# Kernel optimization log

Measured on AMD Instinct MI355X. Metric: run time of the kernel, lower is better.

The kernel has to match this reference:

```python
import jax, jax.numpy as jnp
import numpy as np
from jax import lax

COS_BASIS_NO = 24
SCALE = 6.0
SHIFT = 1.0


def make_kern_basis(T_no):
    # [24, T_no] raised-cosine log-time basis, matching the torch loop exactly
    i = jnp.arange(COS_BASIS_NO, dtype=jnp.float32)
    phi = (jnp.pi / 2.0) * i                                  # [24]
    x = jnp.arange(T_no, dtype=jnp.float32)
    raw = SCALE * jnp.log(x + SHIFT + 1e-7)                   # [T_no]
    basis = 0.5 * jnp.cos(raw[None, :] - phi[:, None]) + 0.5  # [24, T_no]
    inside = (raw[None, :] >= phi[:, None] - jnp.pi) & (raw[None, :] <= phi[:, None] + jnp.pi)
    return jnp.where(inside, basis, 0.0)


def causal_grouped_conv(x, kern, sub_no, T_no):
    # x: [B, sub_no, T], kern: [sub_no*hid, T_no] (already flipped like torch)
    # left-pad T_no-1 zeros == the torch zero-padded buffer; cross-correlation
    rhs = kern[:, None, :]  # OIH with I=1 per group
    return lax.conv_general_dilated(
        x, rhs, window_strides=(1,), padding=[(T_no - 1, 0)],
        feature_group_count=sub_no,
        dimension_numbers=("NCH", "OIH", "NCH"))


def setup_inputs() -> dict:
    key = jax.random.key(0)
    ks = jax.random.split(key, 10)
    B, T_data = 8, 5000
    sub_no, E_no, I_no, T_no, hid_no = 20, 2000, 200, 400, 16
    inp = {
        "S_e": jax.random.uniform(ks[0], (B, T_data, E_no), dtype=jnp.float32),
        "S_i": jax.random.uniform(ks[1], (B, T_data, I_no), dtype=jnp.float32),
        "E_scale": jnp.zeros((E_no,), jnp.float32),
        "I_scale": jnp.zeros((I_no,), jnp.float32),
        "W_e_layer1": jax.random.normal(ks[2], (sub_no * hid_no, COS_BASIS_NO), jnp.float32) * 0.01,
        "W_i_layer1": jax.random.normal(ks[3], (sub_no * hid_no, COS_BASIS_NO), jnp.float32) * 0.01,
        "W_layer2": jnp.full((sub_no, hid_no), -1.0, jnp.float32),
        "b_layer1": jnp.zeros((sub_no * hid_no,), jnp.float32),
        "C_syn_e_raw": jax.random.normal(ks[4], (sub_no, E_no), jnp.float32) * 0.01,
        "C_syn_i_raw": jax.random.normal(ks[5], (sub_no, I_no), jnp.float32) * 0.01,
        "V_o": jnp.zeros((1,), jnp.float32),
        "temp": jnp.asarray(1.0, jnp.float32),
        "T_no": T_no,
        "test": 1,
    }
    return inp


def reference(S_e, S_i, E_scale, I_scale, W_e_layer1, W_i_layer1, W_layer2,
              b_layer1, C_syn_e_raw, C_syn_i_raw, V_o, temp, T_no, test):
    sub_no = C_syn_e_raw.shape[0]
    hid_no = W_layer2.shape[1]
    B, T_data, _ = S_e.shape

    if test:
        C_syn_e = jax.nn.softmax(C_syn_e_raw / temp, axis=0)
        C_syn_i = jax.nn.softmax(C_syn_i_raw / temp, axis=0)
    else:
        eps = 1e-8
        ku, kv = jax.random.split(jax.random.key(42))
        u_e = jax.random.uniform(ku, C_syn_e_raw.shape, dtype=C_syn_e_raw.dtype)
        u_i = jax.random.uniform(kv, C_syn_i_raw.shape, dtype=C_syn_i_raw.dtype)
        g_e = -jnp.log(-jnp.log(u_e + eps) + eps)
        g_i = -jnp.log(-jnp.log(u_i + eps) + eps)
        C_syn_e = jax.nn.softmax((C_syn_e_raw + g_e) / temp, axis=0)
        C_syn_i = jax.nn.softmax((C_syn_i_raw + g_i) / temp, axis=0)

    # scale synapses and project onto subunits: [B,T,E] x [E,sub] -> [B,T,sub]
    syn_e = jnp.einsum("bte,se->bts", S_e * jnp.exp(E_scale)[None, None, :], C_syn_e)
    syn_i = jnp.einsum("bti,si->bts", S_i * jnp.exp(I_scale)[None, None, :], C_syn_i)

    kern_basis = make_kern_basis(T_no)                        # [24, T_no]
    ke = jnp.flip(W_e_layer1 @ kern_basis, axis=1)            # [sub*hid, T_no]
    ki = jnp.flip(W_i_layer1 @ kern_basis, axis=1)

    xe = jnp.transpose(syn_e, (0, 2, 1))                      # [B, sub, T]
    xi = jnp.transpose(syn_i, (0, 2, 1))
    conv_e = causal_grouped_conv(xe, ke, sub_no, T_no)        # [B, sub*hid, T]
    conv_i = causal_grouped_conv(xi, ki, sub_no, T_no)
    layer1 = jnp.tanh(conv_e + conv_i + b_layer1[None, :, None])

    # grouped 1x1 conv == per-subunit weighted reduction over hid
    h = layer1.reshape(B, sub_no, hid_no, T_data)
    sub_out = jnp.einsum("bshT,sh->bTs", h, jnp.exp(W_layer2))  # [B, T, sub]
    final = jnp.sum(sub_out, axis=-1) + V_o                    # [B, T]
    return final, sub_out, C_syn_e, C_syn_i
```

## Files before the change

kernel.cpp:

```cpp
#include <hip/hip_runtime.h>
#include <math.h>

#define PI_F 3.14159265358979323846f
#define BSTRIDE 404

__global__ __launch_bounds__(256) void prep_kernel(
    const float* __restrict__ Ce_raw, const float* __restrict__ Ci_raw,
    const float* __restrict__ Escale, const float* __restrict__ Iscale,
    const float* __restrict__ temp,
    float* __restrict__ CsT_e, float* __restrict__ CsT_i,
    float* __restrict__ basis,
    float* __restrict__ outCe, float* __restrict__ outCi)
{
    int id = blockIdx.x * 256 + threadIdx.x;
    if (id < 2000) {
        int e = id;
        float t = temp[0];
        float v[20];
        float m = -1e30f;
        #pragma unroll
        for (int s = 0; s < 20; ++s) { v[s] = Ce_raw[s * 2000 + e] / t; m = fmaxf(m, v[s]); }
        float sum = 0.f;
        #pragma unroll
        for (int s = 0; s < 20; ++s) { v[s] = expf(v[s] - m); sum += v[s]; }
        float inv = 1.f / sum;
        float sc = expf(Escale[e]);
        #pragma unroll
        for (int s = 0; s < 20; ++s) {
            float p = v[s] * inv;
            outCe[s * 2000 + e] = p;
            CsT_e[e * 20 + s] = p * sc;
        }
    } else if (id < 2200) {
        int e = id - 2000;
        float t = temp[0];
        float v[20];
        float m = -1e30f;
        #pragma unroll
        for (int s = 0; s < 20; ++s) { v[s] = Ci_raw[s * 200 + e] / t; m = fmaxf(m, v[s]); }
        float sum = 0.f;
        #pragma unroll
        for (int s = 0; s < 20; ++s) { v[s] = expf(v[s] - m); sum += v[s]; }
        float inv = 1.f / sum;
        float sc = expf(Iscale[e]);
        #pragma unroll
        for (int s = 0; s < 20; ++s) {
            float p = v[s] * inv;
            outCi[s * 200 + e] = p;
            CsT_i[e * 20 + s] = p * sc;
        }
    } else if (id < 2200 + 24 * BSTRIDE) {
        int idx = id - 2200;
        int j = idx / BSTRIDE, d = idx - j * BSTRIDE;
        float val = 0.f;
        if (d < 400) {
            float raw = 6.0f * logf((float)d + 1.0f + 1e-7f);
            float ph = (PI_F * 0.5f) * (float)j;
            if (raw >= ph - PI_F && raw <= ph + PI_F) val = 0.5f * cosf(raw - ph) + 0.5f;
        }
        basis[idx] = val;
    } else if (id < 11896 + 48) {
        int row = 2000 + (id - 11896);
        #pragma unroll
        for (int s = 0; s < 20; ++s) CsT_e[row * 20 + s] = 0.f;
    } else if (id < 11944 + 56) {
        int row = 200 + (id - 11944);
        #pragma unroll
        for (int s = 0; s < 20; ++s) CsT_i[row * 20 + s] = 0.f;
    }
}

__global__ __launch_bounds__(256) void syn_kernel(
    const float* __restrict__ Se, const float* __restrict__ Si,
    const float* __restrict__ Ce, const float* __restrict__ Ci,
    float* __restrict__ outA, float* __restrict__ outB,
    float* __restrict__ outI)
{
    __shared__ float4 tile[64 * 33];
    float* red = reinterpret_cast<float*>(tile);
    const int tid = threadIdx.x;
    const int lane = tid & 63;
    const int w = __builtin_amdgcn_readfirstlane(tid >> 6);
    const int r0 = blockIdx.x * 64;
    const int z = blockIdx.z;

    const float* S   = (z == 2) ? Si : Se;
    const float* CsT = (z == 2) ? Ci : Ce;
    float* out       = (z == 0) ? outA : (z == 1) ? outB : outI;
    const int Eno    = (z == 2) ? 200 : 2000;
    const int ch0    = (z == 1) ? 8 : 0;
    const int nch    = (z == 2) ? 2 : 8;

    float acc[20];
    #pragma unroll
    for (int s = 0; s < 20; ++s) acc[s] = 0.f;

    for (int cc = 0; cc < nch; ++cc) {
        const int ebase = (ch0 + cc) * 128;
        #pragma unroll
        for (int i = 0; i < 8; ++i) {
            int f = tid + i * 256;
            int row = f >> 5, col4 = f & 31;
            int e0 = ebase + col4 * 4;
            float4 v = make_float4(0.f, 0.f, 0.f, 0.f);
            if (e0 + 4 <= Eno)
                v = *reinterpret_cast<const float4*>(S + (size_t)(r0 + row) * Eno + e0);
            tile[row * 33 + col4] = v;
        }
        __syncthreads();

        const float4* crow = reinterpret_cast<const float4*>(CsT + (size_t)(ebase + w * 32) * 20);
        #pragma unroll
        for (int c4 = 0; c4 < 8; ++c4) {
            float4 v = tile[lane * 33 + w * 8 + c4];
            const float4* ct = crow + c4 * 20;
            float vv[4] = {v.x, v.y, v.z, v.w};
            #pragma unroll
            for (int q = 0; q < 4; ++q) {
                float sv = vv[q];
                #pragma unroll
                for (int c5 = 0; c5 < 5; ++c5) {
                    float4 cc2 = ct[q * 5 + c5];
                    acc[c5 * 4 + 0] = fmaf(sv, cc2.x, acc[c5 * 4 + 0]);
                    acc[c5 * 4 + 1] = fmaf(sv, cc2.y, acc[c5 * 4 + 1]);
                    acc[c5 * 4 + 2] = fmaf(sv, cc2.z, acc[c5 * 4 + 2]);
                    acc[c5 * 4 + 3] = fmaf(sv, cc2.w, acc[c5 * 4 + 3]);
                }
            }
        }
        __syncthreads();
    }

    #pragma unroll
    for (int s = 0; s < 20; ++s) red[(w * 64 + lane) * 21 + s] = acc[s];
    __syncthreads();

    #pragma unroll
    for (int i = 0; i < 5; ++i) {
        int p = tid + i * 256;
        int row = p & 63, s = p >> 6;
        float a = red[(0 * 64 + row) * 21 + s] + red[(1 * 64 + row) * 21 + s]
                + red[(2 * 64 + row) * 21 + s] + red[(3 * 64 + row) * 21 + s];
        int r = r0 + row;
        int b = r / 5000, t = r - b * 5000;
        out[((size_t)b * 20 + s) * 5000 + t] = a;
    }
}

__device__ const int CJ_LO[24] = {0,0,0,0,0,0,0,0,0,4,4,8,12,16,20,28,36,48,64,84,108,140,184,240};
__device__ const int CJ_NB[24] = {1,1,1,1,2,2,3,3,4,4,5,6,7,9,12,15,19,25,31,41,53,65,54,40};

__device__ __forceinline__ int phys4(int g) {
    return (g & ~15) | ((g >> 1) & 7) | ((g & 1) << 3);
}

__global__ __launch_bounds__(128) void conv_kernel(
    const float* __restrict__ syn_eA, const float* __restrict__ syn_eB,
    const float* __restrict__ syn_i, const float* __restrict__ basis,
    const float* __restrict__ W_e, const float* __restrict__ W_i,
    const float* __restrict__ b1, const float* __restrict__ W2,
    float* __restrict__ sub_out)
{
    __shared__ float4 win4[16 + 464];
    float4* wbase = win4 + 16;
    float2* win2 = reinterpret_cast<float2*>(wbase);
    const int tid = threadIdx.x;
    const int tile = blockIdx.x, s = blockIdx.y, bz = blockIdx.z;
    const int t0 = tile * 512;

    const float* seA = syn_eA + ((size_t)bz * 20 + s) * 5000;
    const float* seB = syn_eB + ((size_t)bz * 20 + s) * 5000;
    const float* si  = syn_i  + ((size_t)bz * 20 + s) * 5000;
    for (int l = tid; l < 920; l += 128) {
        int t = t0 - 404 + l;
        float ve = 0.f, vi = 0.f;
        if ((unsigned)t < 5000u) { ve = seA[t] + seB[t]; vi = si[t]; }
        int g = l >> 1;
        win2[2 * phys4(g) + (l & 1)] = make_float2(ve, vi);
    }
    __syncthreads();

    float z[16][4];
    #pragma unroll
    for (int h = 0; h < 16; ++h) {
        float bv = b1[s * 16 + h];
        #pragma unroll
        for (int k = 0; k < 4; ++k) z[h][k] = bv;
    }

    const int base = 4 * tid + 400;

    for (int j = 0; j < 24; ++j) {
        const float4* bj4 = reinterpret_cast<const float4*>(basis + j * BSTRIDE);
        const int lo = CJ_LO[j];
        const int nb = CJ_NB[j];
        const int co = lo >> 2;
        float be0 = 0.f, be1 = 0.f, be2 = 0.f, be3 = 0.f;
        float bi0 = 0.f, bi1 = 0.f, bi2 = 0.f, bi3 = 0.f;

        auto body = [&](const float4& V0, const float4& V1,
                        const float4& V2, const float4& V3, const float4& c) {
            be0 = fmaf(c.x, V2.x, be0); bi0 = fmaf(c.x, V2.y, bi0);
            be1 = fmaf(c.x, V2.z, be1); bi1 = fmaf(c.x, V2.w, bi1);
            be2 = fmaf(c.x, V3.x, be2); bi2 = fmaf(c.x, V3.y, bi2);
            be3 = fmaf(c.x, V3.z, be3); bi3 = fmaf(c.x, V3.w, bi3);
            be0 = fmaf(c.y, V1.z, be0); bi0 = fmaf(c.y, V1.w, bi0);
            be1 = fmaf(c.y, V2.x, be1); bi1 = fmaf(c.y, V2.y, bi1);
            be2 = fmaf(c.y, V2.z, be2); bi2 = fmaf(c.y, V2.w, bi2);
            be3 = fmaf(c.y, V3.x, be3); bi3 = fmaf(c.y, V3.y, bi3);
            be0 = fmaf(c.z, V1.x, be0); bi0 = fmaf(c.z, V1.y, bi0);
            be1 = fmaf(c.z, V1.z, be1); bi1 = fmaf(c.z, V1.w, bi1);
            be2 = fmaf(c.z, V2.x, be2); bi2 = fmaf(c.z, V2.y, bi2);
            be3 = fmaf(c.z, V2.z, be3); bi3 = fmaf(c.z, V2.w, bi3);
            be0 = fmaf(c.w, V0.z, be0); bi0 = fmaf(c.w, V0.w, bi0);
            be1 = fmaf(c.w, V1.x, be1); bi1 = fmaf(c.w, V1.y, bi1);
            be2 = fmaf(c.w, V1.z, be2); bi2 = fmaf(c.w, V1.w, bi2);
            be3 = fmaf(c.w, V2.x, be3); bi3 = fmaf(c.w, V2.y, bi3);
        };

        const int g0 = (base - lo) >> 1;
        auto LP = [&](int n, float4& lo4, float4& hi4) {
            int p = phys4(g0 - 2 * n);
            lo4 = wbase[p]; hi4 = wbase[p + 8];
        };

        float4 A0, A1, B0, B1, C0, C1, D0, D1;
        float4 E0, E1, F0, F1, G0, G1, H0, H1;
        LP(-1, A0, A1); LP(0, B0, B1); LP(1, C0, C1); LP(2, D0, D1);
        float4 cB = bj4[co], cC = bj4[co + 1], cD = bj4[co + 2];

        int bb = 0;
        while (bb + 8 <= nb) {
            LP(bb + 3, E0, E1); float4 cE = bj4[co + bb + 3];
            body(B0, B1, A0, A1, cB);
            LP(bb + 4, F0, F1); float4 cF = bj4[co + bb + 4];
            body(C0, C1, B0, B1, cC);
            LP(bb + 5, G0, G1); float4 cG = bj4[co + bb + 5];
            body(D0, D1, C0, C1, cD);
            LP(bb + 6, H0, H1); float4 cH = bj4[co + bb + 6];
            body(E0, E1, D0, D1, cE);
            LP(bb + 7, A0, A1); float4 cI = bj4[co + bb + 7];
            body(F0, F1, E0, E1, cF);
            LP(bb + 8, B0, B1); cB = bj4[co + bb + 8];
            body(G0, G1, F0, F1, cG);
            LP(bb + 9, C0, C1); cC = bj4[co + bb + 9];
            body(H0, H1, G0, G1, cH);
            LP(bb + 10, D0, D1); cD = bj4[co + bb + 10];
            body(A0, A1, H0, H1, cI);
            bb += 8;
        }
        int r = nb - bb;
        if (r > 0) { body(B0, B1, A0, A1, cB);
          if (r > 1) { body(C0, C1, B0, B1, cC);
            if (r > 2) { body(D0, D1, C0, C1, cD);
              if (r > 3) { LP(bb + 3, E0, E1); float4 cE = bj4[co + bb + 3];
                body(E0, E1, D0, D1, cE);
                if (r > 4) { LP(bb + 4, F0, F1); float4 cF = bj4[co + bb + 4];
                  body(F0, F1, E0, E1, cF);
                  if (r > 5) { LP(bb + 5, G0, G1); float4 cG = bj4[co + bb + 5];
                    body(G0, G1, F0, F1, cG);
                    if (r > 6) { LP(bb + 6, H0, H1); float4 cH = bj4[co + bb + 6];
                      body(H0, H1, G0, G1, cH); } } } } } } }

        #pragma unroll
        for (int h = 0; h < 16; ++h) {
            float we = W_e[(s * 16 + h) * 24 + j];
            float wi = W_i[(s * 16 + h) * 24 + j];
            z[h][0] = fmaf(we, be0, fmaf(wi, bi0, z[h][0]));
            z[h][1] = fmaf(we, be1, fmaf(wi, bi1, z[h][1]));
            z[h][2] = fmaf(we, be2, fmaf(wi, bi2, z[h][2]));
            z[h][3] = fmaf(we, be3, fmaf(wi, bi3, z[h][3]));
        }
    }

    float w2v[16];
    #pragma unroll
    for (int h = 0; h < 16; ++h) w2v[h] = __expf(W2[s * 16 + h]);

    #pragma unroll
    for (int k = 0; k < 4; ++k) {
        int t = t0 + 4 * tid + k;
        if (t < 5000) {
            float acc = 0.f;
            #pragma unroll
            for (int h = 0; h < 16; ++h) {
                float e2 = __expf(2.0f * z[h][k]);
                float th = 1.0f - 2.0f / (e2 + 1.0f);
                acc = fmaf(w2v[h], th, acc);
            }
            sub_out[((size_t)bz * 5000 + t) * 20 + s] = acc;
        }
    }
}

__global__ __launch_bounds__(256) void final_kernel(
    const float* __restrict__ sub_out, const float* __restrict__ V_o,
    float* __restrict__ fin)
{
    int r = blockIdx.x * 256 + threadIdx.x;
    if (r < 40000) {
        const float* p = sub_out + (size_t)r * 20;
        float a = V_o[0];
        #pragma unroll
        for (int s = 0; s < 20; ++s) a += p[s];
        fin[r] = a;
    }
}

extern "C" void kernel_launch(void* const* d_in, const int* in_sizes, int n_in,
                              void* d_out, int out_size, void* d_ws, size_t ws_size,
                              hipStream_t stream)
{
    const float* S_e     = (const float*)d_in[0];
    const float* S_i     = (const float*)d_in[1];
    const float* E_scale = (const float*)d_in[2];
    const float* I_scale = (const float*)d_in[3];
    const float* W_e     = (const float*)d_in[4];
    const float* W_i     = (const float*)d_in[5];
    const float* W2      = (const float*)d_in[6];
    const float* b1      = (const float*)d_in[7];
    const float* Ce_raw  = (const float*)d_in[8];
    const float* Ci_raw  = (const float*)d_in[9];
    const float* V_o     = (const float*)d_in[10];
    const float* temp    = (const float*)d_in[11];

    float* out     = (float*)d_out;
    float* fin     = out;
    float* sub_out = out + 40000;
    float* outCe   = out + 840000;
    float* outCi   = out + 880000;

    float* ws     = (float*)d_ws;
    float* CsT_e  = ws;
    float* CsT_i  = ws + 40960;
    float* basis  = ws + 46080;
    float* syn_eA = ws + 55776;
    float* syn_eB = ws + 855776;
    float* syn_i  = ws + 1655776;

    prep_kernel<<<47, 256, 0, stream>>>(Ce_raw, Ci_raw, E_scale, I_scale, temp,
                                        CsT_e, CsT_i, basis, outCe, outCi);
    syn_kernel<<<dim3(625, 1, 3), 256, 0, stream>>>(S_e, S_i, CsT_e, CsT_i,
                                                    syn_eA, syn_eB, syn_i);
    conv_kernel<<<dim3(10, 20, 8), 128, 0, stream>>>(syn_eA, syn_eB, syn_i, basis,
                                                     W_e, W_i, b1, W2, sub_out);
    final_kernel<<<157, 256, 0, stream>>>(sub_out, V_o, fin);
}
```

Before: 300.9 us.

## Double-buffer synapse tiles with register prefetch in syn_kernel

Reworks the syn_kernel reduction loop to use two smaller shared-memory tiles of 64 columns each, with global loads for the next two chunks prefetched into registers while the current chunk is computed. This is meant to hide global-memory latency behind the FMA work instead of stalling on a load-then-sync per chunk. It costs extra registers for the prefetch buffers and twice as many barriers per column processed.

```diff
diff --git a/kernel.cpp b/kernel.cpp
--- a/kernel.cpp
+++ b/kernel.cpp
@@ -76,7 +76,7 @@
     float* __restrict__ outA, float* __restrict__ outB,
     float* __restrict__ outI)
 {
-    __shared__ float4 tile[64 * 33];
+    __shared__ float4 tile[2][64 * 17];
     float* red = reinterpret_cast<float*>(tile);
     const int tid = threadIdx.x;
     const int lane = tid & 63;
@@ -88,48 +88,69 @@
     const float* CsT = (z == 2) ? Ci : Ce;
     float* out       = (z == 0) ? outA : (z == 1) ? outB : outI;
     const int Eno    = (z == 2) ? 200 : 2000;
-    const int ch0    = (z == 1) ? 8 : 0;
-    const int nch    = (z == 2) ? 2 : 8;
+    const int eb0    = (z == 1) ? 1024 : 0;
+    const int nch    = (z == 2) ? 4 : 16;
 
     float acc[20];
     #pragma unroll
     for (int s = 0; s < 20; ++s) acc[s] = 0.f;
 
-    for (int cc = 0; cc < nch; ++cc) {
-        const int ebase = (ch0 + cc) * 128;
-        #pragma unroll
-        for (int i = 0; i < 8; ++i) {
-            int f = tid + i * 256;
-            int row = f >> 5, col4 = f & 31;
-            int e0 = ebase + col4 * 4;
-            float4 v = make_float4(0.f, 0.f, 0.f, 0.f);
-            if (e0 + 4 <= Eno)
-                v = *reinterpret_cast<const float4*>(S + (size_t)(r0 + row) * Eno + e0);
-            tile[row * 33 + col4] = v;
-        }
-        __syncthreads();
-
-        const float4* crow = reinterpret_cast<const float4*>(CsT + (size_t)(ebase + w * 32) * 20);
-        #pragma unroll
-        for (int c4 = 0; c4 < 8; ++c4) {
-            float4 v = tile[lane * 33 + w * 8 + c4];
-            const float4* ct = crow + c4 * 20;
+    const int frow = tid >> 4, fcol = tid & 15;
+
+    auto ldG = [&](int ch, float4 (&v)[4]) {
+        const int eb = eb0 + ch * 64;
+        #pragma unroll
+        for (int i = 0; i < 4; ++i) {
+            int row = frow + i * 16;
+            int e0 = eb + fcol * 4;
+            v[i] = make_float4(0.f, 0.f, 0.f, 0.f);
+            if (ch < nch && e0 + 4 <= Eno)
+                v[i] = *reinterpret_cast<const float4*>(S + (size_t)(r0 + row) * Eno + e0);
+        }
+    };
+    auto put = [&](int buf, float4 (&v)[4]) {
+        #pragma unroll
+        for (int i = 0; i < 4; ++i)
+            tile[buf][(frow + i * 16) * 17 + fcol] = v[i];
+    };
+    auto compute = [&](int buf, int ch) {
+        const int eb = eb0 + ch * 64;
+        const float4* crow = reinterpret_cast<const float4*>(CsT) + (size_t)(eb + w * 16) * 5;
+        #pragma unroll
+        for (int c4 = 0; c4 < 4; ++c4) {
+            float4 v = tile[buf][lane * 17 + w * 4 + c4];
             float vv[4] = {v.x, v.y, v.z, v.w};
             #pragma unroll
             for (int q = 0; q < 4; ++q) {
+                const float4* ct = crow + (c4 * 4 + q) * 5;
                 float sv = vv[q];
                 #pragma unroll
                 for (int c5 = 0; c5 < 5; ++c5) {
-                    float4 cc2 = ct[q * 5 + c5];
-                    acc[c5 * 4 + 0] = fmaf(sv, cc2.x, acc[c5 * 4 + 0]);
-                    acc[c5 * 4 + 1] = fmaf(sv, cc2.y, acc[c5 * 4 + 1]);
-                    acc[c5 * 4 + 2] = fmaf(sv, cc2.z, acc[c5 * 4 + 2]);
-                    acc[c5 * 4 + 3] = fmaf(sv, cc2.w, acc[c5 * 4 + 3]);
+                    float4 cc = ct[c5];
+                    acc[c5 * 4 + 0] = fmaf(sv, cc.x, acc[c5 * 4 + 0]);
+                    acc[c5 * 4 + 1] = fmaf(sv, cc.y, acc[c5 * 4 + 1]);
+                    acc[c5 * 4 + 2] = fmaf(sv, cc.z, acc[c5 * 4 + 2]);
+                    acc[c5 * 4 + 3] = fmaf(sv, cc.w, acc[c5 * 4 + 3]);
                 }
             }
         }
+    };
+
+    float4 A[4], B[4];
+    ldG(0, A); ldG(1, B);
+    put(0, A);
+
+    for (int ch = 0; ch < nch; ch += 2) {
+        ldG(ch + 2, A);
         __syncthreads();
-    }
+        compute(0, ch);
+        put(1, B);
+        ldG(ch + 3, B);
+        __syncthreads();
+        compute(1, ch + 1);
+        put(0, A);
+    }
+    __syncthreads();
 
     #pragma unroll
     for (int s = 0; s < 20; ++s) red[(w * 64 + lane) * 21 + s] = acc[s];
```

New measurement: 312.5 us. +3.9%, slower.
